# Optimization experiments

Measured on AMD Instinct MI355X. Metric: run time of the kernel, lower is better.

Reference implementation:

```python
import jax, jax.numpy as jnp
import numpy as np

B, H, S, D = 4, 16, 2048, 64
SCALE_FACTOR = 8.0  # forward arg; module multiplies qk by 1/scale_factor = 0.125 = 1/sqrt(D)
# dropout_p is an undefined global in the source module; treated as 0 (identity)
# for a deterministic reference.

def setup_inputs() -> dict:
    key0 = jax.random.key(0)
    kq, kk, kv = jax.random.split(key0, 3)
    query = jax.random.normal(kq, (B, H, S, D), dtype=jnp.float32)
    key = jax.random.normal(kk, (B, H, S, D), dtype=jnp.float32)
    value = jax.random.normal(kv, (B, H, S, D), dtype=jnp.float32)
    return {"query": query, "key": key, "value": value}

def reference(query, key, value):
    inv_scale = 1.0 / SCALE_FACTOR
    # [B,H,S,S] attention scores (the module materializes this full matrix)
    qk = jnp.einsum('bhqd,bhkd->bhqk', query, key) * inv_scale
    probs = jax.nn.softmax(qk, axis=-1)
    # dropout is identity (p effectively 0 / eval-mode deterministic baseline)
    out = jnp.einsum('bhqk,bhkd->bhqd', probs, value)
    return out
```

## Files before the change

### kernel.cpp

```cpp
#include <hip/hip_runtime.h>
#include <hip/hip_bf16.h>

#define SEQ 2048
#define DIMH 64
#define KB 64
#define NT (SEQ / KB)

typedef __attribute__((ext_vector_type(8))) short bf16x8;
typedef __attribute__((ext_vector_type(4))) float f32x4;

extern "C" __device__ float __ocml_native_exp2_f32(float);
#define EXP2(x) __ocml_native_exp2_f32(x)

__device__ inline unsigned short f2bf(float f) {
    union { __bf16 h; unsigned short u; } c;
    c.h = (__bf16)f;
    return c.u;
}
__device__ inline unsigned pack2(float a, float b) {
    return (unsigned)f2bf(a) | ((unsigned)f2bf(b) << 16);
}

__device__ inline int swz(int row, int col) {
    int g = (((row & 7) ^ ((row >> 3) & 7)) << 3);
    return row * 64 + (col ^ g);
}

__device__ inline void perm32swap(unsigned &a, unsigned &b) {
    asm("v_permlane32_swap_b32 %0, %1" : "+v"(a), "+v"(b));
}
__device__ inline void perm16swap(unsigned &a, unsigned &b) {
    asm("v_permlane16_swap_b32 %0, %1" : "+v"(a), "+v"(b));
}

__global__ __launch_bounds__(256, 2) void fattn(
    const float* __restrict__ Q, const float* __restrict__ K,
    const float* __restrict__ V, float* __restrict__ O)
{
    __shared__ __align__(16) unsigned short Ksh[2][KB * DIMH];
    __shared__ __align__(16) unsigned short Vt[2][KB * DIMH];

    const int tid  = threadIdx.x;
    const int lane = tid & 63;
    const int wv   = tid >> 6;

    const int bid = blockIdx.x;
    const int swb = (bid & 7) * 64 + (bid >> 3);
    const int bh  = swb >> 3;
    const int qt  = swb & 7;

    const int l15 = lane & 15;
    const int lg  = lane >> 4;

    const float* qh = Q + (size_t)bh * SEQ * DIMH;
    const float* kh = K + (size_t)bh * SEQ * DIMH;
    const float* vh = V + (size_t)bh * SEQ * DIMH;
    float*       oh = O + (size_t)bh * SEQ * DIMH;

    const int q0 = qt * 256 + wv * 64;

    int koff[4][2];
    #pragma unroll
    for (int n = 0; n < 4; ++n)
        #pragma unroll
        for (int ks = 0; ks < 2; ++ks)
            koff[n][ks] = swz(n * 16 + l15, ks * 32 + lg * 8);

    const int c4 = (tid & 15) * 4;
    const int rK = tid >> 4;
    int kstoff[4], vstoff[4];
    #pragma unroll
    for (int rr = 0; rr < 4; ++rr) kstoff[rr] = swz(rr * 16 + rK, c4);
    #pragma unroll
    for (int j = 0; j < 4; ++j) vstoff[j] = swz(c4 + j, rK * 4);

    const float QS = 0.180336880111120f;
    bf16x8 qf[4][2];
    #pragma unroll
    for (int h = 0; h < 4; ++h)
        #pragma unroll
        for (int ks = 0; ks < 2; ++ks) {
            const float* src = qh + (size_t)(q0 + h * 16 + l15) * DIMH + ks * 32 + lg * 8;
            f32x4 a = *reinterpret_cast<const f32x4*>(src);
            f32x4 b = *reinterpret_cast<const f32x4*>(src + 4);
            bf16x8 vq;
            #pragma unroll
            for (int j = 0; j < 4; ++j) {
                vq[j]     = (short)f2bf(a[j] * QS);
                vq[j + 4] = (short)f2bf(b[j] * QS);
            }
            qf[h][ks] = vq;
        }

    bf16x8 ones;
    #pragma unroll
    for (int j = 0; j < 8; ++j) ones[j] = (short)0x3F80;

    f32x4 oacc[4][4];
    #pragma unroll
    for (int h = 0; h < 4; ++h)
        #pragma unroll
        for (int d = 0; d < 4; ++d) oacc[h][d] = (f32x4){0.f, 0.f, 0.f, 0.f};
    f32x4 lacc[4] = {{0.f,0.f,0.f,0.f}, {0.f,0.f,0.f,0.f},
                     {0.f,0.f,0.f,0.f}, {0.f,0.f,0.f,0.f}};

    {
        #pragma unroll
        for (int rr = 0; rr < 4; ++rr) {
            const f32x4 k4 = *reinterpret_cast<const f32x4*>(
                kh + (size_t)(rr * 16 + rK) * DIMH + c4);
            uint2 kk;
            kk.x = pack2(k4[0], k4[1]);
            kk.y = pack2(k4[2], k4[3]);
            *reinterpret_cast<uint2*>(&Ksh[0][kstoff[rr]]) = kk;
        }
        f32x4 v4[4];
        #pragma unroll
        for (int i = 0; i < 4; ++i)
            v4[i] = *reinterpret_cast<const f32x4*>(
                vh + (size_t)(rK * 4 + i) * DIMH + c4);
        #pragma unroll
        for (int j = 0; j < 4; ++j) {
            uint2 w;
            w.x = pack2(v4[0][j], v4[1][j]);
            w.y = pack2(v4[2][j], v4[3][j]);
            *reinterpret_cast<uint2*>(&Vt[0][vstoff[j]]) = w;
        }
    }
    __syncthreads();

    for (int kt = 0; kt < NT; ++kt) {
        const int cur = kt & 1;
        const int nxt = cur ^ 1;
        const unsigned short* Kb = Ksh[cur];
        const unsigned short* Vb = Vt[cur];
        const bool pf = (kt + 1 < NT);

        if (pf) {
            const size_t tb = (size_t)(kt + 1) * KB;
            #pragma unroll
            for (int rr = 0; rr < 4; ++rr) {
                const f32x4 k4 = *reinterpret_cast<const f32x4*>(
                    kh + (tb + rr * 16 + rK) * DIMH + c4);
                uint2 kk;
                kk.x = pack2(k4[0], k4[1]);
                kk.y = pack2(k4[2], k4[3]);
                *reinterpret_cast<uint2*>(&Ksh[nxt][kstoff[rr]]) = kk;
            }
            f32x4 v4[4];
            #pragma unroll
            for (int i = 0; i < 4; ++i)
                v4[i] = *reinterpret_cast<const f32x4*>(
                    vh + (tb + rK * 4 + i) * DIMH + c4);
            #pragma unroll
            for (int j = 0; j < 4; ++j) {
                uint2 w;
                w.x = pack2(v4[0][j], v4[1][j]);
                w.y = pack2(v4[2][j], v4[3][j]);
                *reinterpret_cast<uint2*>(&Vt[nxt][vstoff[j]]) = w;
            }
        }

        __builtin_amdgcn_s_setprio(1);

        bf16x8 pa[4][2];
        #pragma unroll
        for (int np = 0; np < 2; ++np) {
            unsigned u[4][4];
            #pragma unroll
            for (int nn = 0; nn < 2; ++nn) {
                const int n = np * 2 + nn;
                bf16x8 kf0 = *reinterpret_cast<const bf16x8*>(&Kb[koff[n][0]]);
                bf16x8 kf1 = *reinterpret_cast<const bf16x8*>(&Kb[koff[n][1]]);
                #pragma unroll
                for (int h = 0; h < 4; ++h) {
                    f32x4 a = {0.f, 0.f, 0.f, 0.f};
                    a = __builtin_amdgcn_mfma_f32_16x16x32_bf16(kf0, qf[h][0], a, 0, 0, 0);
                    a = __builtin_amdgcn_mfma_f32_16x16x32_bf16(kf1, qf[h][1], a, 0, 0, 0);
                    u[h][2 * nn]     = pack2(EXP2(a[0]), EXP2(a[1]));
                    u[h][2 * nn + 1] = pack2(EXP2(a[2]), EXP2(a[3]));
                }
            }
            #pragma unroll
            for (int h = 0; h < 4; ++h) {
                unsigned a0 = u[h][0], b0 = u[h][2];
                unsigned a1 = u[h][1], b1 = u[h][3];
                perm32swap(a0, b0); perm16swap(a0, b0);
                perm32swap(a1, b1); perm16swap(a1, b1);
                union { unsigned w[4]; bf16x8 v; } pu;
                pu.w[0] = a0; pu.w[1] = a1; pu.w[2] = b0; pu.w[3] = b1;
                pa[h][np] = pu.v;
            }
        }

        #pragma unroll
        for (int h = 0; h < 4; ++h) {
            lacc[h] = __builtin_amdgcn_mfma_f32_16x16x32_bf16(pa[h][0], ones, lacc[h], 0, 0, 0);
            lacc[h] = __builtin_amdgcn_mfma_f32_16x16x32_bf16(pa[h][1], ones, lacc[h], 0, 0, 0);
        }

        #pragma unroll
        for (int d = 0; d < 4; ++d) {
            bf16x8 vb0 = *reinterpret_cast<const bf16x8*>(&Vb[koff[d][0]]);
            bf16x8 vb1 = *reinterpret_cast<const bf16x8*>(&Vb[koff[d][1]]);
            #pragma unroll
            for (int h = 0; h < 4; ++h) {
                oacc[h][d] = __builtin_amdgcn_mfma_f32_16x16x32_bf16(pa[h][0], vb0, oacc[h][d], 0, 0, 0);
                oacc[h][d] = __builtin_amdgcn_mfma_f32_16x16x32_bf16(pa[h][1], vb1, oacc[h][d], 0, 0, 0);
            }
        }

        __builtin_amdgcn_s_setprio(0);

        if (pf) {
            asm volatile("s_waitcnt lgkmcnt(0)" ::: "memory");
            __builtin_amdgcn_s_barrier();
            asm volatile("" ::: "memory");
        }
    }

    #pragma unroll
    for (int h = 0; h < 4; ++h)
        #pragma unroll
        for (int r = 0; r < 4; ++r) {
            float inv = 1.0f / lacc[h][r];
            float* dst = oh + (size_t)(q0 + h * 16 + lg * 4 + r) * DIMH;
            #pragma unroll
            for (int d = 0; d < 4; ++d)
                dst[d * 16 + l15] = oacc[h][d][r] * inv;
        }
}

extern "C" void kernel_launch(void* const* d_in, const int* in_sizes, int n_in,
                              void* d_out, int out_size, void* d_ws, size_t ws_size,
                              hipStream_t stream) {
    const float* q = (const float*)d_in[0];
    const float* k = (const float*)d_in[1];
    const float* v = (const float*)d_in[2];
    float* out = (float*)d_out;
    dim3 grid(64 * (SEQ / 256));
    dim3 block(256);
    fattn<<<grid, block, 0, stream>>>(q, k, v, out);
}
```

Baseline: 91.83 us.

## Halve workgroup size to 128 threads with 128-query tiles and doubled grid

Each workgroup now handles 128 queries with 2 waves instead of 256 queries with 4 waves, so the grid doubles to 1024 blocks. Each thread stages twice as many K/V rows into LDS per tile to make up for the fewer threads. The block-index swizzle is remapped to match. This improves load balance and CU fill across the 256 CUs. The cost is that each K/V tile is loaded and converted by twice as many workgroups, which doubles global K/V traffic and staging work per query.

```diff
diff --git a/kernel.cpp b/kernel.cpp
--- a/kernel.cpp
+++ b/kernel.cpp
@@ -33,7 +33,7 @@
     asm("v_permlane16_swap_b32 %0, %1" : "+v"(a), "+v"(b));
 }
 
-__global__ __launch_bounds__(256, 2) void fattn(
+__global__ __launch_bounds__(128, 2) void fattn(
     const float* __restrict__ Q, const float* __restrict__ K,
     const float* __restrict__ V, float* __restrict__ O)
 {
@@ -45,9 +45,9 @@
     const int wv   = tid >> 6;
 
     const int bid = blockIdx.x;
-    const int swb = (bid & 7) * 64 + (bid >> 3);
-    const int bh  = swb >> 3;
-    const int qt  = swb & 7;
+    const int swb = (bid & 7) * 128 + (bid >> 3);
+    const int bh  = swb >> 4;
+    const int qt  = swb & 15;
 
     const int l15 = lane & 15;
     const int lg  = lane >> 4;
@@ -57,7 +57,7 @@
     const float* vh = V + (size_t)bh * SEQ * DIMH;
     float*       oh = O + (size_t)bh * SEQ * DIMH;
 
-    const int q0 = qt * 256 + wv * 64;
+    const int q0 = qt * 128 + wv * 64;
 
     int koff[4][2];
     #pragma unroll
@@ -68,11 +68,14 @@
 
     const int c4 = (tid & 15) * 4;
     const int rK = tid >> 4;
-    int kstoff[4], vstoff[4];
-    #pragma unroll
-    for (int rr = 0; rr < 4; ++rr) kstoff[rr] = swz(rr * 16 + rK, c4);
-    #pragma unroll
-    for (int j = 0; j < 4; ++j) vstoff[j] = swz(c4 + j, rK * 4);
+    int kstoff[8], vstoff[2][4];
+    #pragma unroll
+    for (int rr = 0; rr < 8; ++rr) kstoff[rr] = swz(rr * 8 + rK, c4);
+    #pragma unroll
+    for (int a = 0; a < 2; ++a)
+        #pragma unroll
+        for (int j = 0; j < 4; ++j)
+            vstoff[a][j] = swz(c4 + j, a * 32 + rK * 4);
 
     const float QS = 0.180336880111120f;
     bf16x8 qf[4][2];
@@ -104,62 +107,44 @@
     f32x4 lacc[4] = {{0.f,0.f,0.f,0.f}, {0.f,0.f,0.f,0.f},
                      {0.f,0.f,0.f,0.f}, {0.f,0.f,0.f,0.f}};
 
-    {
-        #pragma unroll
-        for (int rr = 0; rr < 4; ++rr) {
+    auto stage_tile = [&](int t, int b) {
+        const size_t tb = (size_t)t * KB;
+        #pragma unroll
+        for (int rr = 0; rr < 8; ++rr) {
             const f32x4 k4 = *reinterpret_cast<const f32x4*>(
-                kh + (size_t)(rr * 16 + rK) * DIMH + c4);
+                kh + (tb + rr * 8 + rK) * DIMH + c4);
             uint2 kk;
             kk.x = pack2(k4[0], k4[1]);
             kk.y = pack2(k4[2], k4[3]);
-            *reinterpret_cast<uint2*>(&Ksh[0][kstoff[rr]]) = kk;
-        }
-        f32x4 v4[4];
-        #pragma unroll
-        for (int i = 0; i < 4; ++i)
-            v4[i] = *reinterpret_cast<const f32x4*>(
-                vh + (size_t)(rK * 4 + i) * DIMH + c4);
-        #pragma unroll
-        for (int j = 0; j < 4; ++j) {
-            uint2 w;
-            w.x = pack2(v4[0][j], v4[1][j]);
-            w.y = pack2(v4[2][j], v4[3][j]);
-            *reinterpret_cast<uint2*>(&Vt[0][vstoff[j]]) = w;
-        }
-    }
-    __syncthreads();
-
-    for (int kt = 0; kt < NT; ++kt) {
-        const int cur = kt & 1;
-        const int nxt = cur ^ 1;
-        const unsigned short* Kb = Ksh[cur];
-        const unsigned short* Vb = Vt[cur];
-        const bool pf = (kt + 1 < NT);
-
-        if (pf) {
-            const size_t tb = (size_t)(kt + 1) * KB;
-            #pragma unroll
-            for (int rr = 0; rr < 4; ++rr) {
-                const f32x4 k4 = *reinterpret_cast<const f32x4*>(
-                    kh + (tb + rr * 16 + rK) * DIMH + c4);
-                uint2 kk;
-                kk.x = pack2(k4[0], k4[1]);
-                kk.y = pack2(k4[2], k4[3]);
-                *reinterpret_cast<uint2*>(&Ksh[nxt][kstoff[rr]]) = kk;
-            }
+            *reinterpret_cast<uint2*>(&Ksh[b][kstoff[rr]]) = kk;
+        }
+        #pragma unroll
+        for (int a = 0; a < 2; ++a) {
             f32x4 v4[4];
             #pragma unroll
             for (int i = 0; i < 4; ++i)
                 v4[i] = *reinterpret_cast<const f32x4*>(
-                    vh + (tb + rK * 4 + i) * DIMH + c4);
+                    vh + (tb + a * 32 + rK * 4 + i) * DIMH + c4);
             #pragma unroll
             for (int j = 0; j < 4; ++j) {
                 uint2 w;
                 w.x = pack2(v4[0][j], v4[1][j]);
                 w.y = pack2(v4[2][j], v4[3][j]);
-                *reinterpret_cast<uint2*>(&Vt[nxt][vstoff[j]]) = w;
-            }
-        }
+                *reinterpret_cast<uint2*>(&Vt[b][vstoff[a][j]]) = w;
+            }
+        }
+    };
+
+    stage_tile(0, 0);
+    __syncthreads();
+
+    for (int kt = 0; kt < NT; ++kt) {
+        const int cur = kt & 1;
+        const unsigned short* Kb = Ksh[cur];
+        const unsigned short* Vb = Vt[cur];
+        const bool pf = (kt + 1 < NT);
+
+        if (pf) stage_tile(kt + 1, cur ^ 1);
 
         __builtin_amdgcn_s_setprio(1);
 
@@ -238,7 +223,7 @@
     const float* k = (const float*)d_in[1];
     const float* v = (const float*)d_in[2];
     float* out = (float*)d_out;
-    dim3 grid(64 * (SEQ / 256));
-    dim3 block(256);
+    dim3 grid(64 * (SEQ / 128));
+    dim3 block(128);
     fattn<<<grid, block, 0, stream>>>(q, k, v, out);
 }
```

Measured after the change: 102.2 us. 1.11x slower.

## Split KV range across two blocks with workspace partials and combine kernel

Applied to the files above, without the earlier changes.

Each query tile's key/value range is split into two halves processed by separate blocks. Each block writes unnormalized partial outputs and row sums to a workspace, and a second kernel sums the halves and divides. The aim is more blocks for parallelism and load balance, at the cost of significant extra global memory traffic and a second launch. It falls back to the original single kernel if the workspace is too small.

```diff
diff --git a/kernel.cpp b/kernel.cpp
--- a/kernel.cpp
+++ b/kernel.cpp
@@ -4,7 +4,10 @@
 #define SEQ 2048
 #define DIMH 64
 #define KB 64
-#define NT (SEQ / KB)
+#define NHEADS 64
+#define NT_FULL (SEQ / KB)
+#define HALF_KV (SEQ / 2)
+#define NT_HALF (HALF_KV / KB)
 
 typedef __attribute__((ext_vector_type(8))) short bf16x8;
 typedef __attribute__((ext_vector_type(4))) float f32x4;
@@ -33,9 +36,10 @@
     asm("v_permlane16_swap_b32 %0, %1" : "+v"(a), "+v"(b));
 }
 
-__global__ __launch_bounds__(256, 2) void fattn(
+__global__ __launch_bounds__(256, 2) void fattn_part(
     const float* __restrict__ Q, const float* __restrict__ K,
-    const float* __restrict__ V, float* __restrict__ O)
+    const float* __restrict__ V, float* __restrict__ wsO,
+    float* __restrict__ wsL)
 {
     __shared__ __align__(16) unsigned short Ksh[2][KB * DIMH];
     __shared__ __align__(16) unsigned short Vt[2][KB * DIMH];
@@ -44,10 +48,12 @@
     const int lane = tid & 63;
     const int wv   = tid >> 6;
 
-    const int bid = blockIdx.x;
-    const int swb = (bid & 7) * 64 + (bid >> 3);
-    const int bh  = swb >> 3;
-    const int qt  = swb & 7;
+    const int bid  = blockIdx.x;
+    const int swb  = (bid & 7) * 128 + (bid >> 3);
+    const int bh   = swb >> 4;
+    const int rest = swb & 15;
+    const int qt   = rest >> 1;
+    const int half = rest & 1;
 
     const int l15 = lane & 15;
     const int lg  = lane >> 4;
@@ -55,7 +61,6 @@
     const float* qh = Q + (size_t)bh * SEQ * DIMH;
     const float* kh = K + (size_t)bh * SEQ * DIMH;
     const float* vh = V + (size_t)bh * SEQ * DIMH;
-    float*       oh = O + (size_t)bh * SEQ * DIMH;
 
     const int q0 = qt * 256 + wv * 64;
 
@@ -104,62 +109,42 @@
     f32x4 lacc[4] = {{0.f,0.f,0.f,0.f}, {0.f,0.f,0.f,0.f},
                      {0.f,0.f,0.f,0.f}, {0.f,0.f,0.f,0.f}};
 
-    {
+    auto stage_tile = [&](int t, int b) {
+        const size_t tb = (size_t)t * KB;
         #pragma unroll
         for (int rr = 0; rr < 4; ++rr) {
             const f32x4 k4 = *reinterpret_cast<const f32x4*>(
-                kh + (size_t)(rr * 16 + rK) * DIMH + c4);
+                kh + (tb + rr * 16 + rK) * DIMH + c4);
             uint2 kk;
             kk.x = pack2(k4[0], k4[1]);
             kk.y = pack2(k4[2], k4[3]);
-            *reinterpret_cast<uint2*>(&Ksh[0][kstoff[rr]]) = kk;
+            *reinterpret_cast<uint2*>(&Ksh[b][kstoff[rr]]) = kk;
         }
         f32x4 v4[4];
         #pragma unroll
         for (int i = 0; i < 4; ++i)
             v4[i] = *reinterpret_cast<const f32x4*>(
-                vh + (size_t)(rK * 4 + i) * DIMH + c4);
+                vh + (tb + rK * 4 + i) * DIMH + c4);
         #pragma unroll
         for (int j = 0; j < 4; ++j) {
             uint2 w;
             w.x = pack2(v4[0][j], v4[1][j]);
             w.y = pack2(v4[2][j], v4[3][j]);
-            *reinterpret_cast<uint2*>(&Vt[0][vstoff[j]]) = w;
-        }
-    }
+            *reinterpret_cast<uint2*>(&Vt[b][vstoff[j]]) = w;
+        }
+    };
+
+    const int tile0 = half * NT_HALF;
+    stage_tile(tile0, 0);
     __syncthreads();
 
-    for (int kt = 0; kt < NT; ++kt) {
+    for (int kt = 0; kt < NT_HALF; ++kt) {
         const int cur = kt & 1;
-        const int nxt = cur ^ 1;
         const unsigned short* Kb = Ksh[cur];
         const unsigned short* Vb = Vt[cur];
-        const bool pf = (kt + 1 < NT);
-
-        if (pf) {
-            const size_t tb = (size_t)(kt + 1) * KB;
-            #pragma unroll
-            for (int rr = 0; rr < 4; ++rr) {
-                const f32x4 k4 = *reinterpret_cast<const f32x4*>(
-                    kh + (tb + rr * 16 + rK) * DIMH + c4);
-                uint2 kk;
-                kk.x = pack2(k4[0], k4[1]);
-                kk.y = pack2(k4[2], k4[3]);
-                *reinterpret_cast<uint2*>(&Ksh[nxt][kstoff[rr]]) = kk;
-            }
-            f32x4 v4[4];
-            #pragma unroll
-            for (int i = 0; i < 4; ++i)
-                v4[i] = *reinterpret_cast<const f32x4*>(
-                    vh + (tb + rK * 4 + i) * DIMH + c4);
-            #pragma unroll
-            for (int j = 0; j < 4; ++j) {
-                uint2 w;
-                w.x = pack2(v4[0][j], v4[1][j]);
-                w.y = pack2(v4[2][j], v4[3][j]);
-                *reinterpret_cast<uint2*>(&Vt[nxt][vstoff[j]]) = w;
-            }
-        }
+        const bool pf = (kt + 1 < NT_HALF);
+
+        if (pf) stage_tile(tile0 + kt + 1, cur ^ 1);
 
         __builtin_amdgcn_s_setprio(1);
 
@@ -219,6 +204,210 @@
         }
     }
 
+    float* op = wsO + (size_t)half * ((size_t)NHEADS * SEQ * DIMH)
+                    + ((size_t)bh * SEQ + q0) * DIMH;
+    #pragma unroll
+    for (int h = 0; h < 4; ++h)
+        #pragma unroll
+        for (int r = 0; r < 4; ++r) {
+            float* dst = op + (size_t)(h * 16 + lg * 4 + r) * DIMH;
+            #pragma unroll
+            for (int d = 0; d < 4; ++d)
+                dst[d * 16 + l15] = oacc[h][d][r];
+        }
+    if (l15 == 0) {
+        float* lp = wsL + (size_t)half * (NHEADS * SEQ) + (size_t)bh * SEQ + q0;
+        #pragma unroll
+        for (int h = 0; h < 4; ++h)
+            #pragma unroll
+            for (int r = 0; r < 4; ++r)
+                lp[h * 16 + lg * 4 + r] = lacc[h][r];
+    }
+}
+
+__global__ __launch_bounds__(256) void fattn_combine(
+    const float* __restrict__ wsO, const float* __restrict__ wsL,
+    float* __restrict__ out)
+{
+    const int total4 = NHEADS * SEQ * DIMH / 4;
+    const int stride = gridDim.x * blockDim.x;
+    for (int i4 = blockIdx.x * blockDim.x + threadIdx.x; i4 < total4; i4 += stride) {
+        const int qg = i4 >> 4;
+        const float inv = 1.0f / (wsL[qg] + wsL[NHEADS * SEQ + qg]);
+        const f32x4 a = reinterpret_cast<const f32x4*>(wsO)[i4];
+        const f32x4 b = reinterpret_cast<const f32x4*>(wsO)[total4 + i4];
+        f32x4 r;
+        #pragma unroll
+        for (int j = 0; j < 4; ++j) r[j] = (a[j] + b[j]) * inv;
+        reinterpret_cast<f32x4*>(out)[i4] = r;
+    }
+}
+
+__global__ __launch_bounds__(256, 2) void fattn_full(
+    const float* __restrict__ Q, const float* __restrict__ K,
+    const float* __restrict__ V, float* __restrict__ O)
+{
+    __shared__ __align__(16) unsigned short Ksh[2][KB * DIMH];
+    __shared__ __align__(16) unsigned short Vt[2][KB * DIMH];
+
+    const int tid  = threadIdx.x;
+    const int lane = tid & 63;
+    const int wv   = tid >> 6;
+
+    const int bid = blockIdx.x;
+    const int swb = (bid & 7) * 64 + (bid >> 3);
+    const int bh  = swb >> 3;
+    const int qt  = swb & 7;
+
+    const int l15 = lane & 15;
+    const int lg  = lane >> 4;
+
+    const float* qh = Q + (size_t)bh * SEQ * DIMH;
+    const float* kh = K + (size_t)bh * SEQ * DIMH;
+    const float* vh = V + (size_t)bh * SEQ * DIMH;
+    float*       oh = O + (size_t)bh * SEQ * DIMH;
+
+    const int q0 = qt * 256 + wv * 64;
+
+    int koff[4][2];
+    #pragma unroll
+    for (int n = 0; n < 4; ++n)
+        #pragma unroll
+        for (int ks = 0; ks < 2; ++ks)
+            koff[n][ks] = swz(n * 16 + l15, ks * 32 + lg * 8);
+
+    const int c4 = (tid & 15) * 4;
+    const int rK = tid >> 4;
+    int kstoff[4], vstoff[4];
+    #pragma unroll
+    for (int rr = 0; rr < 4; ++rr) kstoff[rr] = swz(rr * 16 + rK, c4);
+    #pragma unroll
+    for (int j = 0; j < 4; ++j) vstoff[j] = swz(c4 + j, rK * 4);
+
+    const float QS = 0.180336880111120f;
+    bf16x8 qf[4][2];
+    #pragma unroll
+    for (int h = 0; h < 4; ++h)
+        #pragma unroll
+        for (int ks = 0; ks < 2; ++ks) {
+            const float* src = qh + (size_t)(q0 + h * 16 + l15) * DIMH + ks * 32 + lg * 8;
+            f32x4 a = *reinterpret_cast<const f32x4*>(src);
+            f32x4 b = *reinterpret_cast<const f32x4*>(src + 4);
+            bf16x8 vq;
+            #pragma unroll
+            for (int j = 0; j < 4; ++j) {
+                vq[j]     = (short)f2bf(a[j] * QS);
+                vq[j + 4] = (short)f2bf(b[j] * QS);
+            }
+            qf[h][ks] = vq;
+        }
+
+    bf16x8 ones;
+    #pragma unroll
+    for (int j = 0; j < 8; ++j) ones[j] = (short)0x3F80;
+
+    f32x4 oacc[4][4];
+    #pragma unroll
+    for (int h = 0; h < 4; ++h)
+        #pragma unroll
+        for (int d = 0; d < 4; ++d) oacc[h][d] = (f32x4){0.f, 0.f, 0.f, 0.f};
+    f32x4 lacc[4] = {{0.f,0.f,0.f,0.f}, {0.f,0.f,0.f,0.f},
+                     {0.f,0.f,0.f,0.f}, {0.f,0.f,0.f,0.f}};
+
+    auto stage_tile = [&](int t, int b) {
+        const size_t tb = (size_t)t * KB;
+        #pragma unroll
+        for (int rr = 0; rr < 4; ++rr) {
+            const f32x4 k4 = *reinterpret_cast<const f32x4*>(
+                kh + (tb + rr * 16 + rK) * DIMH + c4);
+            uint2 kk;
+            kk.x = pack2(k4[0], k4[1]);
+            kk.y = pack2(k4[2], k4[3]);
+            *reinterpret_cast<uint2*>(&Ksh[b][kstoff[rr]]) = kk;
+        }
+        f32x4 v4[4];
+        #pragma unroll
+        for (int i = 0; i < 4; ++i)
+            v4[i] = *reinterpret_cast<const f32x4*>(
+                vh + (tb + rK * 4 + i) * DIMH + c4);
+        #pragma unroll
+        for (int j = 0; j < 4; ++j) {
+            uint2 w;
+            w.x = pack2(v4[0][j], v4[1][j]);
+            w.y = pack2(v4[2][j], v4[3][j]);
+            *reinterpret_cast<uint2*>(&Vt[b][vstoff[j]]) = w;
+        }
+    };
+
+    stage_tile(0, 0);
+    __syncthreads();
+
+    for (int kt = 0; kt < NT_FULL; ++kt) {
+        const int cur = kt & 1;
+        const unsigned short* Kb = Ksh[cur];
+        const unsigned short* Vb = Vt[cur];
+        const bool pf = (kt + 1 < NT_FULL);
+
+        if (pf) stage_tile(kt + 1, cur ^ 1);
+
+        __builtin_amdgcn_s_setprio(1);
+
+        bf16x8 pa[4][2];
+        #pragma unroll
+        for (int np = 0; np < 2; ++np) {
+            unsigned u[4][4];
+            #pragma unroll
+            for (int nn = 0; nn < 2; ++nn) {
+                const int n = np * 2 + nn;
+                bf16x8 kf0 = *reinterpret_cast<const bf16x8*>(&Kb[koff[n][0]]);
+                bf16x8 kf1 = *reinterpret_cast<const bf16x8*>(&Kb[koff[n][1]]);
+                #pragma unroll
+                for (int h = 0; h < 4; ++h) {
+                    f32x4 a = {0.f, 0.f, 0.f, 0.f};
+                    a = __builtin_amdgcn_mfma_f32_16x16x32_bf16(kf0, qf[h][0], a, 0, 0, 0);
+                    a = __builtin_amdgcn_mfma_f32_16x16x32_bf16(kf1, qf[h][1], a, 0, 0, 0);
+                    u[h][2 * nn]     = pack2(EXP2(a[0]), EXP2(a[1]));
+                    u[h][2 * nn + 1] = pack2(EXP2(a[2]), EXP2(a[3]));
+                }
+            }
+            #pragma unroll
+            for (int h = 0; h < 4; ++h) {
+                unsigned a0 = u[h][0], b0 = u[h][2];
+                unsigned a1 = u[h][1], b1 = u[h][3];
+                perm32swap(a0, b0); perm16swap(a0, b0);
+                perm32swap(a1, b1); perm16swap(a1, b1);
+                union { unsigned w[4]; bf16x8 v; } pu;
+                pu.w[0] = a0; pu.w[1] = a1; pu.w[2] = b0; pu.w[3] = b1;
+                pa[h][np] = pu.v;
+            }
+        }
+
+        #pragma unroll
+        for (int h = 0; h < 4; ++h) {
+            lacc[h] = __builtin_amdgcn_mfma_f32_16x16x32_bf16(pa[h][0], ones, lacc[h], 0, 0, 0);
+            lacc[h] = __builtin_amdgcn_mfma_f32_16x16x32_bf16(pa[h][1], ones, lacc[h], 0, 0, 0);
+        }
+
+        #pragma unroll
+        for (int d = 0; d < 4; ++d) {
+            bf16x8 vb0 = *reinterpret_cast<const bf16x8*>(&Vb[koff[d][0]]);
+            bf16x8 vb1 = *reinterpret_cast<const bf16x8*>(&Vb[koff[d][1]]);
+            #pragma unroll
+            for (int h = 0; h < 4; ++h) {
+                oacc[h][d] = __builtin_amdgcn_mfma_f32_16x16x32_bf16(pa[h][0], vb0, oacc[h][d], 0, 0, 0);
+                oacc[h][d] = __builtin_amdgcn_mfma_f32_16x16x32_bf16(pa[h][1], vb1, oacc[h][d], 0, 0, 0);
+            }
+        }
+
+        __builtin_amdgcn_s_setprio(0);
+
+        if (pf) {
+            asm volatile("s_waitcnt lgkmcnt(0)" ::: "memory");
+            __builtin_amdgcn_s_barrier();
+            asm volatile("" ::: "memory");
+        }
+    }
+
     #pragma unroll
     for (int h = 0; h < 4; ++h)
         #pragma unroll
@@ -238,7 +427,17 @@
     const float* k = (const float*)d_in[1];
     const float* v = (const float*)d_in[2];
     float* out = (float*)d_out;
-    dim3 grid(64 * (SEQ / 256));
-    dim3 block(256);
-    fattn<<<grid, block, 0, stream>>>(q, k, v, out);
-}
+
+    const size_t nO = (size_t)2 * NHEADS * SEQ * DIMH;
+    const size_t nL = (size_t)2 * NHEADS * SEQ;
+    const size_t need = (nO + nL) * sizeof(float);
+
+    if (ws_size >= need) {
+        float* wsO = (float*)d_ws;
+        float* wsL = wsO + nO;
+        fattn_part<<<dim3(NHEADS * 16), dim3(256), 0, stream>>>(q, k, v, wsO, wsL);
+        fattn_combine<<<dim3(2048), dim3(256), 0, stream>>>(wsO, wsL, out);
+    } else {
+        fattn_full<<<dim3(NHEADS * (SEQ / 256)), dim3(256), 0, stream>>>(q, k, v, out);
+    }
+}
```

Result: slower. 112.8 us (+22.8%).
